# Kernel optimization log

Hardware: AMD Instinct MI355X
Metric: run time of the kernel (lower is better)

The kernel has to match this reference:

```python
import jax, jax.numpy as jnp
import numpy as np

B, CIN, H, W = 32, 10, 128, 128
APP, WIDTH, M1, M2 = 2, 64, 20, 20
NQ, NP, OUT, MID = 4, 2, 1, 128
LIFT = WIDTH - CIN - APP - NQ  # 48


def setup_inputs() -> dict:
    key = jax.random.key(0)
    ks = jax.random.split(key, 16)
    n = lambda k, s: jax.random.normal(k, s, dtype=jnp.float32)
    sc = 1.0 / (WIDTH * WIDTH)  # FNO spectral weight scale 1/(in*out)
    return {
        'x': n(ks[0], (B, CIN, H, W)),
        'qa': n(ks[1], (NQ, CIN + APP)) * 0.1,
        'qb': n(ks[2], (NQ, CIN + APP)) * 0.1,
        'fc0_w1': n(ks[3], (MID, CIN + APP + NQ)) * 0.1,
        'fc0_b1': jnp.zeros((MID,), jnp.float32),
        'fc0_w2': n(ks[4], (LIFT, MID)) * 0.1,
        'fc0_b2': jnp.zeros((LIFT,), jnp.float32),
        'sw1r': n(ks[5], (4, WIDTH, WIDTH, M1, M2)) * sc,
        'sw1i': n(ks[6], (4, WIDTH, WIDTH, M1, M2)) * sc,
        'sw2r': n(ks[7], (4, WIDTH, WIDTH, M1, M2)) * sc,
        'sw2i': n(ks[8], (4, WIDTH, WIDTH, M1, M2)) * sc,
        'cw': n(ks[9], (4, WIDTH, WIDTH, 3, 3)) * 0.05,
        'cb': jnp.zeros((4, WIDTH), jnp.float32),
        'pw': n(ks[10], (4, WIDTH, 2 * WIDTH + NP)) * 0.05,
        'pb': jnp.zeros((4, WIDTH), jnp.float32),
        'fc1_w1': n(ks[11], (MID, WIDTH)) * 0.1,
        'fc1_b1': jnp.zeros((MID,), jnp.float32),
        'fc1_w2': n(ks[12], (OUT, MID)) * 0.1,
        'fc1_b2': jnp.zeros((OUT,), jnp.float32),
    }


def _conv1x1(x, w, b):
    # x: (B,C,H,W), w: (O,C), b: (O,)
    return jnp.einsum('oc,bchw->bohw', w, x) + b[None, :, None, None]


def _spectral_conv(x, w1, w2):
    # standard FNO2d spectral conv: keep low modes in both rfft corners
    xf = jnp.fft.rfft2(x)                                  # (B,C,H,W//2+1) complex
    top = jnp.einsum('bixy,ioxy->boxy', xf[:, :, :M1, :M2], w1)
    bot = jnp.einsum('bixy,ioxy->boxy', xf[:, :, -M1:, :M2], w2)
    of = jnp.zeros((x.shape[0], WIDTH, H, W // 2 + 1), dtype=xf.dtype)
    of = of.at[:, :, :M1, :M2].set(top).at[:, :, -M1:, :M2].set(bot)
    return jnp.fft.irfft2(of, s=(H, W))


def _circ_conv3(x, w, b):
    # Conv2d(k=3, padding=1, padding_mode='circular')
    xp = jnp.pad(x, ((0, 0), (0, 0), (1, 1), (1, 1)), mode='wrap')
    y = jax.lax.conv_general_dilated(xp, w, (1, 1), 'VALID',
                                     dimension_numbers=('NCHW', 'OIHW', 'NCHW'))
    return y + b[None, :, None, None]


def _grid(b, h, w):
    gx = jnp.broadcast_to(jnp.linspace(0.0, 1.0, h, dtype=jnp.float32)[None, None, :, None], (b, 1, h, w))
    gy = jnp.broadcast_to(jnp.linspace(0.0, 1.0, w, dtype=jnp.float32)[None, None, None, :], (b, 1, h, w))
    return jnp.concatenate([gx, gy], axis=1)


def reference(x, qa, qb, fc0_w1, fc0_b1, fc0_w2, fc0_b2,
              sw1r, sw1i, sw2r, sw2i, cw, cb, pw, pb,
              fc1_w1, fc1_b1, fc1_w2, fc1_b2):
    b = x.shape[0]
    x = jnp.concatenate([x, _grid(b, H, W)], axis=1)            # (B, 12, H, W)
    # QuadPath (prep stage): product of two learned linear projections
    q = jnp.einsum('oc,bchw->bohw', qa, x) * jnp.einsum('oc,bchw->bohw', qb, x)
    x = jnp.concatenate([x, q], axis=1)                          # (B, 16, H, W)
    # fc0 lift MLP (1x1 conv -> gelu -> 1x1 conv), concat to reach width
    h0 = jax.nn.gelu(_conv1x1(x, fc0_w1, fc0_b1))
    x = jnp.concatenate([x, _conv1x1(h0, fc0_w2, fc0_b2)], axis=1)  # (B, 64, H, W)

    for i in range(4):
        x1 = _spectral_conv(x, sw1r[i] + 1j * sw1i[i], sw2r[i] + 1j * sw2i[i])
        x2 = _circ_conv3(x, cw[i], cb[i])
        xo = jnp.concatenate([x1, x2], axis=1)                   # (B, 128, H, W)
        prods = xo[:, :NP] * xo[:, NP:2 * NP]                     # ProductLayer pair products
        xo = _conv1x1(jnp.concatenate([xo, prods], axis=1), pw[i], pb[i])
        x = x + jnp.tanh(xo)

    h1 = jax.nn.gelu(_conv1x1(x, fc1_w1, fc1_b1))
    return _conv1x1(h1, fc1_w2, fc1_b2)                          # (B, 1, H, W)
```

## Files before the change

kernel.cpp:

```cpp
#include <hip/hip_runtime.h>
#include <math.h>

#define HW 16384

typedef __attribute__((ext_vector_type(8))) short short8;
typedef __attribute__((ext_vector_type(4))) float f32x4;
typedef unsigned int u32;

__device__ __forceinline__ float gelu_tanh(float x) {
    float x3 = x * x * x;
    float t = tanhf(0.7978845608028654f * (x + 0.044715f * x3));
    return 0.5f * x * (1.0f + t);
}

__device__ __forceinline__ u32 f2bf(float f) {
    u32 u = __builtin_bit_cast(u32, f);
    return (u + 0x7FFFu + ((u >> 16) & 1u)) >> 16;
}
__device__ __forceinline__ u32 pack2(float a, float b) {
    return f2bf(a) | (f2bf(b) << 16);
}

__global__ __launch_bounds__(256) void packw_kernel(
    const float* __restrict__ cw, short* __restrict__ wpk)
{
    int idx = blockIdx.x * 256 + threadIdx.x;
    if (idx >= 4 * 64 * 576) return;
    int L = idx / 36864, r = idx % 36864;
    int o = r / 576, k = r % 576;
    int tap = k >> 6, i = k & 63;
    wpk[idx] = (short)f2bf(cw[((size_t)(L * 64 + o) * 64 + i) * 9 + tap]);
}
__global__ __launch_bounds__(256) void packpw_kernel(
    const float* __restrict__ pw, short* __restrict__ pwk)
{
    int idx = blockIdx.x * 256 + threadIdx.x;
    if (idx >= 4 * 64 * 128) return;
    int L = idx >> 13, r = idx & 8191;
    int o = r >> 7, k = r & 127;
    pwk[idx] = (short)f2bf(pw[(size_t)L * 8320 + o * 130 + k]);
}
__global__ __launch_bounds__(256) void packfc_kernel(
    const float* __restrict__ fc0w1, const float* __restrict__ fc0w2,
    const float* __restrict__ fc1w1,
    short* __restrict__ w1k, short* __restrict__ w2k, short* __restrict__ f1wk)
{
    int i = blockIdx.x * 256 + threadIdx.x;
    if (i < 4096) {
        int m = i >> 5, k = i & 31;
        w1k[i] = (short)(k < 16 ? f2bf(fc0w1[m * 16 + k]) : 0);
    } else if (i < 10240) {
        int j = i - 4096; int o = j >> 7, m = j & 127;
        w2k[j] = (short)f2bf(fc0w2[o * 128 + m]);
    } else if (i < 18432) {
        int j = i - 10240; int m = j >> 6, c = j & 63;
        f1wk[j] = (short)f2bf(fc1w1[m * 64 + c]);
    }
}
__global__ __launch_bounds__(256) void packsw_kernel(
    const float* __restrict__ sw1r, const float* __restrict__ sw1i,
    const float* __restrict__ sw2r, const float* __restrict__ sw2i,
    u32* __restrict__ wswk)
{
    __shared__ short lr[64][202];
    __shared__ short li[64][202];
    int bi = blockIdx.x;
    int L = bi >> 7, i = (bi >> 1) & 63, kh = bi & 1;
    int t = threadIdx.x;
    int km0 = kh * 200;
    for (int region = 0; region < 2; ++region) {
        const float* srcR = region ? sw2r : sw1r;
        const float* srcI = region ? sw2i : sw1i;
        size_t sb = ((size_t)(L * 64 + i) * 64) * 400 + km0;
        for (int c = 0; c < 50; ++c) {
            int flat = c * 256 + t;
            int o = flat / 200, km = flat - o * 200;
            lr[o][km] = (short)f2bf(srcR[sb + (size_t)o * 400 + km]);
            li[o][km] = (short)f2bf(srcI[sb + (size_t)o * 400 + km]);
        }
        __syncthreads();
        u32* dst = wswk + ((size_t)L * 800 + (size_t)region * 400 + km0) * 4096 + (size_t)i * 64;
        for (int c = 0; c < 50; ++c) {
            int flat = c * 256 + t;
            int km = flat >> 6, o = flat & 63;
            dst[(size_t)km * 4096 + o] =
                (u32)(unsigned short)lr[o][km] | ((u32)(unsigned short)li[o][km] << 16);
        }
        __syncthreads();
    }
}
__global__ __launch_bounds__(256) void gen_dft_kernel(
    short* __restrict__ Wfg, short* __restrict__ Winvbg,
    short* __restrict__ Tfy, short* __restrict__ Tiy)
{
    int idx = blockIdx.x * 256 + threadIdx.x;
    if (idx < 6144) {
        int n = idx >> 7, xx = idx & 127;
        float val = 0.f;
        if (n < 40) {
            int kx = n >> 1;
            float s, c;
            sincosf(6.283185307179586f * (float)((kx * xx) & 127) / 128.0f, &s, &c);
            val = (n & 1) ? -s : c;
        }
        Wfg[idx] = (short)f2bf(val);
    } else if (idx < 14336) {
        int j = idx - 6144;
        int xx = j >> 6, k = j & 63;
        float val = 0.f;
        if (k < 40) {
            int kx = k >> 1;
            if (kx == 0) {
                val = (k & 1) ? 0.f : (1.0f / 16384.0f);
            } else {
                float s, c;
                sincosf(6.283185307179586f * (float)((kx * xx) & 127) / 128.0f, &s, &c);
                val = ((k & 1) ? -s : c) * (2.0f / 16384.0f);
            }
        }
        Winvbg[j] = (short)f2bf(val);
    } else if (idx < 24576) {
        int j = idx - 14336;
        int q = j >> 7, yy = j & 127;
        int kyi = q >> 1;
        int ky = kyi + ((kyi >= 20) ? 88 : 0);
        float s, c;
        sincosf(6.283185307179586f * (float)((ky * yy) & 127) / 128.0f, &s, &c);
        Tfy[j] = (short)f2bf((q & 1) ? s : c);
    } else if (idx < 36864) {
        int j = idx - 24576;
        int yy = j / 96, q = j - yy * 96;
        float val = 0.f;
        if (q < 80) {
            int kyi = q >> 1;
            int ky = kyi + ((kyi >= 20) ? 88 : 0);
            float s, c;
            sincosf(6.283185307179586f * (float)((ky * yy) & 127) / 128.0f, &s, &c);
            val = (q & 1) ? s : c;
        }
        Tiy[j] = (short)f2bf(val);
    }
}

__global__ __launch_bounds__(256) void front_mfma_kernel(
    const float* __restrict__ x,
    const float* __restrict__ qa, const float* __restrict__ qb,
    const short* __restrict__ w1k, const float* __restrict__ b1,
    const short* __restrict__ w2k, const float* __restrict__ b2,
    float* __restrict__ xbuf, short* __restrict__ xb16)
{
    __shared__ short V[128 * 40];
    __shared__ short A2[128 * 136];
    __shared__ float lqa[48], lqb[48], lb1[128], lb2[48];
    int t = threadIdx.x;
    int y = blockIdx.x, b = blockIdx.y;
    int lane = t & 63, w = t >> 6;

    if (t < 48) { lqa[t] = qa[t]; lqb[t] = qb[t]; lb2[t] = b2[t]; }
    if (t >= 128) lb1[t - 128] = b1[t - 128];
    __syncthreads();

    if (t < 128) {
        int xx = t;
        float v[16];
        const float* xsrc = x + (size_t)b * 10 * HW + y * 128 + xx;
#pragma unroll
        for (int c = 0; c < 10; ++c) v[c] = xsrc[c * HW];
        v[10] = (float)y * (1.0f / 127.0f);
        v[11] = (float)xx * (1.0f / 127.0f);
#pragma unroll
        for (int o = 0; o < 4; ++o) {
            float sa = 0.f, sb = 0.f;
#pragma unroll
            for (int c = 0; c < 12; ++c) { sa += lqa[o * 12 + c] * v[c]; sb += lqb[o * 12 + c] * v[c]; }
            v[12 + o] = sa * sb;
        }
        u32* vr = (u32*)&V[xx * 40];
#pragma unroll
        for (int j = 0; j < 8; ++j) vr[j] = pack2(v[2 * j], v[2 * j + 1]);
#pragma unroll
        for (int j = 8; j < 16; ++j) vr[j] = 0u;
        float* ob = xbuf + (size_t)b * 64 * HW + y * 128 + xx;
#pragma unroll
        for (int c = 0; c < 16; ++c) ob[(size_t)c * HW] = v[c];
        u32* hb = (u32*)&xb16[(((size_t)b * 128 + y) * 128 + xx) * 64];
#pragma unroll
        for (int j = 0; j < 8; ++j) hb[j] = vr[j];
    }
    __syncthreads();

    {
        short8 aF[2];
#pragma unroll
        for (int mi = 0; mi < 2; ++mi)
            aF[mi] = *(const short8*)(w1k + ((w * 2 + mi) * 16 + (lane & 15)) * 32 + (lane >> 4) * 8);
        f32x4 acc[2][8];
#pragma unroll
        for (int mi = 0; mi < 2; ++mi)
#pragma unroll
            for (int nf = 0; nf < 8; ++nf) acc[mi][nf] = (f32x4){0.f, 0.f, 0.f, 0.f};
#pragma unroll
        for (int nf = 0; nf < 8; ++nf) {
            int xx = nf * 16 + (lane & 15);
            short8 bF = *(const short8*)&V[xx * 40 + (lane >> 4) * 8];
#pragma unroll
            for (int mi = 0; mi < 2; ++mi)
                acc[mi][nf] = __builtin_amdgcn_mfma_f32_16x16x32_bf16(aF[mi], bF, acc[mi][nf], 0, 0, 0);
        }
#pragma unroll
        for (int mi = 0; mi < 2; ++mi) {
            int m0 = (w * 2 + mi) * 16 + (lane >> 4) * 4;
            float bb0 = lb1[m0], bb1 = lb1[m0 + 1], bb2 = lb1[m0 + 2], bb3 = lb1[m0 + 3];
#pragma unroll
            for (int nf = 0; nf < 8; ++nf) {
                int xx = nf * 16 + (lane & 15);
                float h0 = gelu_tanh(acc[mi][nf][0] + bb0);
                float h1 = gelu_tanh(acc[mi][nf][1] + bb1);
                float h2 = gelu_tanh(acc[mi][nf][2] + bb2);
                float h3 = gelu_tanh(acc[mi][nf][3] + bb3);
                *(int2*)&A2[xx * 136 + m0] = make_int2(pack2(h0, h1), pack2(h2, h3));
            }
        }
    }
    __syncthreads();

    {
        short8 aF[3][4];
#pragma unroll
        for (int mt = 0; mt < 3; ++mt)
#pragma unroll
            for (int ks = 0; ks < 4; ++ks)
                aF[mt][ks] = *(const short8*)(w2k + (mt * 16 + (lane & 15)) * 128 + ks * 32 + (lane >> 4) * 8);
#pragma unroll
        for (int ni = 0; ni < 2; ++ni) {
            int nt = w * 2 + ni;
            int xx = nt * 16 + (lane & 15);
            f32x4 acc[3];
#pragma unroll
            for (int mt = 0; mt < 3; ++mt) acc[mt] = (f32x4){0.f, 0.f, 0.f, 0.f};
#pragma unroll
            for (int ks = 0; ks < 4; ++ks) {
                short8 bF = *(const short8*)&A2[xx * 136 + ks * 32 + (lane >> 4) * 8];
#pragma unroll
                for (int mt = 0; mt < 3; ++mt)
                    acc[mt] = __builtin_amdgcn_mfma_f32_16x16x32_bf16(aF[mt][ks], bF, acc[mt], 0, 0, 0);
            }
#pragma unroll
            for (int mt = 0; mt < 3; ++mt) {
                int o0 = mt * 16 + (lane >> 4) * 4;
                float r0 = acc[mt][0] + lb2[o0], r1 = acc[mt][1] + lb2[o0 + 1];
                float r2 = acc[mt][2] + lb2[o0 + 2], r3 = acc[mt][3] + lb2[o0 + 3];
                float* ob = xbuf + (size_t)b * 64 * HW + (size_t)(16 + o0) * HW + y * 128 + xx;
                ob[0] = r0; ob[HW] = r1; ob[2 * HW] = r2; ob[3 * HW] = r3;
                *(int2*)&xb16[(((size_t)b * 128 + y) * 128 + xx) * 64 + 16 + o0] =
                    make_int2(pack2(r0, r1), pack2(r2, r3));
            }
        }
    }
}

__global__ __launch_bounds__(256) void dftfwd_kernel(
    const float* __restrict__ xin, const short* __restrict__ Wfg,
    const short* __restrict__ Tfy, float2* __restrict__ fm)
{
    __shared__ short img[128 * 128];
    __shared__ short S[48 * 140];
    int t = threadIdx.x;
    int bc = blockIdx.x;
    int lane = t & 63, w = t >> 6;

    const float* src = xin + (size_t)bc * HW;
#pragma unroll
    for (int i = 0; i < 8; ++i) {
        int chunk = i * 256 + t;
        int y = chunk >> 4, x8 = chunk & 15;
        const float* p = src + y * 128 + x8 * 8;
        f32x4 v0 = *(const f32x4*)p, v1 = *(const f32x4*)(p + 4);
        int4 h = make_int4(pack2(v0[0], v0[1]), pack2(v0[2], v0[3]),
                           pack2(v1[0], v1[1]), pack2(v1[2], v1[3]));
        *(int4*)&img[y * 128 + ((x8 ^ (y & 7)) << 3)] = h;
    }
    for (int z = t; z < 560; z += 256) ((u32*)S)[2800 + z] = 0u;

    short8 bF[3][4];
#pragma unroll
    for (int nf = 0; nf < 3; ++nf)
#pragma unroll
        for (int ks = 0; ks < 4; ++ks) {
            int n = nf * 16 + (lane & 15);
            bF[nf][ks] = *(const short8*)(Wfg + n * 128 + ks * 32 + (lane >> 4) * 8);
        }
    __syncthreads();

    {
        f32x4 acc[2][3];
#pragma unroll
        for (int a = 0; a < 2; ++a)
#pragma unroll
            for (int b2 = 0; b2 < 3; ++b2) acc[a][b2] = (f32x4){0.f, 0.f, 0.f, 0.f};
#pragma unroll
        for (int ks = 0; ks < 4; ++ks)
#pragma unroll
            for (int mf = 0; mf < 2; ++mf) {
                int y = w * 32 + mf * 16 + (lane & 15);
                int x0 = ks * 32 + (lane >> 4) * 8;
                short8 aF = *(const short8*)&img[y * 128 + ((((x0 >> 3) ^ (y & 7))) << 3)];
#pragma unroll
                for (int nf = 0; nf < 3; ++nf)
                    acc[mf][nf] = __builtin_amdgcn_mfma_f32_16x16x32_bf16(aF, bF[nf][ks], acc[mf][nf], 0, 0, 0);
            }
#pragma unroll
        for (int mf = 0; mf < 2; ++mf)
#pragma unroll
            for (int nf = 0; nf < 3; ++nf) {
                int n = nf * 16 + (lane & 15);
                if (n < 40) {
                    int y0 = w * 32 + mf * 16 + (lane >> 4) * 4;
                    *(int2*)&S[n * 140 + y0] = make_int2(pack2(acc[mf][nf][0], acc[mf][nf][1]),
                                                         pack2(acc[mf][nf][2], acc[mf][nf][3]));
                }
            }
    }
    __syncthreads();

    float2* fmo = fm + (size_t)bc * 800;
#pragma unroll
    for (int pi = 0; pi < 4; ++pi) {
        int p = w + pi * 4;
        if (p < 15) {
            int mt = p / 3, nt = p % 3;
            f32x4 acc = (f32x4){0.f, 0.f, 0.f, 0.f};
#pragma unroll
            for (int ks = 0; ks < 4; ++ks) {
                short8 aF = *(const short8*)(Tfy + (mt * 16 + (lane & 15)) * 128 + ks * 32 + (lane >> 4) * 8);
                short8 bG = *(const short8*)&S[(nt * 16 + (lane & 15)) * 140 + ks * 32 + (lane >> 4) * 8];
                acc = __builtin_amdgcn_mfma_f32_16x16x32_bf16(aF, bG, acc, 0, 0, 0);
            }
            float p0 = __shfl_xor(acc[0], 1), p1 = __shfl_xor(acc[1], 1);
            float p2 = __shfl_xor(acc[2], 1), p3 = __shfl_xor(acc[3], 1);
            int l15 = lane & 15;
            if (!(l15 & 1)) {
                int kx = nt * 8 + (l15 >> 1);
                if (kx < 20) {
                    int kyi0 = mt * 8 + ((lane >> 4) << 1);
                    fmo[kyi0 * 20 + kx] = make_float2(acc[0] + p1, p0 - acc[1]);
                    fmo[(kyi0 + 1) * 20 + kx] = make_float2(acc[2] + p3, p2 - acc[3]);
                }
            }
        }
    }
}

__global__ __launch_bounds__(256) void specmul_kernel(
    const float2* __restrict__ fm,
    const u32* __restrict__ wswk,
    float2* __restrict__ fm2, int nb64)
{
    __shared__ float2 lx[32 * 64];
    __shared__ u32 lw[64 * 64];
    int t = threadIdx.x;
    int mode = blockIdx.x;
    const u32* ws = wswk + (size_t)mode * 4096;
    for (int n = t; n < nb64; n += 256)
        lx[n] = fm[(size_t)n * 800 + mode];
    for (int n = t; n < 4096; n += 256)
        lw[n] = ws[n];
    __syncthreads();
    for (int n = t; n < nb64; n += 256) {
        int b = n >> 6, o = n & 63;
        float re = 0.f, imv = 0.f;
        const float2* xb = lx + b * 64;
#pragma unroll 8
        for (int i = 0; i < 64; ++i) {
            float2 a = xb[i];
            u32 wp = lw[i * 64 + o];
            float wr = __builtin_bit_cast(float, wp << 16);
            float wi = __builtin_bit_cast(float, wp & 0xffff0000u);
            re += a.x * wr - a.y * wi;
            imv += a.x * wi + a.y * wr;
        }
        fm2[(size_t)n * 800 + mode] = make_float2(re, imv);
    }
}

__global__ __launch_bounds__(256) void invA_mfma_kernel(
    const float2* __restrict__ fm2, const short* __restrict__ Tiy,
    short* __restrict__ g)
{
    __shared__ short F[48 * 104];
    int t = threadIdx.x;
    int bc = blockIdx.x;
    int lane = t & 63, w = t >> 6;
    int bb = bc >> 6, cc = bc & 63;
    u32* Fw = (u32*)F;
    const float2* src = fm2 + (size_t)bc * 800;
    for (int i = t; i < 800; i += 256) {
        float2 v = src[i];
        int kyi = i / 20, kx = i - kyi * 20;
        Fw[(2 * kx) * 52 + kyi]     = pack2(v.x, -v.y);
        Fw[(2 * kx + 1) * 52 + kyi] = pack2(v.y, v.x);
    }
    for (int i = t; i < 416; i += 256) Fw[2080 + i] = 0u;
    for (int i = t; i < 384; i += 256) {
        int n = i >> 3, k = i & 7;
        Fw[n * 52 + 40 + k] = 0u;
    }
    __syncthreads();

    short8 aF[3][3];
#pragma unroll
    for (int mt = 0; mt < 3; ++mt)
#pragma unroll
        for (int ks = 0; ks < 3; ++ks)
            aF[mt][ks] = *(const short8*)&F[(mt * 16 + (lane & 15)) * 104 + ks * 32 + (lane >> 4) * 8];

#pragma unroll
    for (int ni = 0; ni < 2; ++ni) {
        int nt = w * 2 + ni;
        int yy = nt * 16 + (lane & 15);
        short8 bF[3];
#pragma unroll
        for (int ks = 0; ks < 3; ++ks)
            bF[ks] = *(const short8*)(Tiy + yy * 96 + ks * 32 + (lane >> 4) * 8);
#pragma unroll
        for (int mt = 0; mt < 3; ++mt) {
            f32x4 acc = (f32x4){0.f, 0.f, 0.f, 0.f};
#pragma unroll
            for (int ks = 0; ks < 3; ++ks)
                acc = __builtin_amdgcn_mfma_f32_16x16x32_bf16(aF[mt][ks], bF[ks], acc, 0, 0, 0);
            int n0 = mt * 16 + (lane >> 4) * 4;
            *(int2*)&g[(((size_t)bb * 128 + yy) * 64 + cc) * 48 + n0] =
                make_int2(pack2(acc[0], acc[1]), pack2(acc[2], acc[3]));
        }
    }
}

__global__ __launch_bounds__(256) void invBcomb_kernel(
    const short* __restrict__ g,
    const short* __restrict__ Winvbg,
    const short* __restrict__ c2g,
    const short* __restrict__ pwk,
    const float* __restrict__ pw,
    const float* __restrict__ pb,
    float* __restrict__ xio,
    short* __restrict__ xb16)
{
    __shared__ short A[64 * 64];
    __shared__ short S1[128 * 64];
    __shared__ short C2[128 * 64];
    __shared__ float2 pr[128];
    int t = threadIdx.x;
    int y = blockIdx.x;
    int b = blockIdx.y;
    int lane = t & 63, w = t >> 6;
    short8 vz = {0, 0, 0, 0, 0, 0, 0, 0};

    {
        const short* gb = g + ((size_t)(b * 128 + y)) * 64 * 48;
#pragma unroll
        for (int i = 0; i < 2; ++i) {
            int chunk = i * 256 + t;
            int c = chunk >> 3, g8 = chunk & 7;
            short8 v = (g8 < 6) ? *(const short8*)(gb + c * 48 + g8 * 8) : vz;
            *(short8*)&A[(c << 6) + ((g8 ^ (c & 7)) << 3)] = v;
        }
    }
    {
        const short* c2b = c2g + ((size_t)(b * 128 + y)) * 128 * 64;
#pragma unroll
        for (int i = 0; i < 4; ++i) {
            int chunk = i * 256 + t;
            int xx = chunk >> 3, c8 = chunk & 7;
            *(short8*)&C2[xx * 64 + ((c8 ^ (xx & 7)) << 3)] = *(const short8*)(c2b + chunk * 8);
        }
    }
    short8 bFi[8][2];
#pragma unroll
    for (int nf = 0; nf < 8; ++nf)
#pragma unroll
        for (int ks = 0; ks < 2; ++ks) {
            int xx = nf * 16 + (lane & 15);
            bFi[nf][ks] = *(const short8*)(Winvbg + xx * 64 + ks * 32 + (lane >> 4) * 8);
        }
    __syncthreads();

    {
        int c0 = w * 16;
        int c = c0 + (lane & 15);
        int base = c << 6;
        short8 aF0 = *(const short8*)&A[base + (((lane >> 4) ^ (c & 7)) << 3)];
        short8 aF1 = *(const short8*)&A[base + (((4 + (lane >> 4)) ^ (c & 7)) << 3)];
        int cw = c0 + (lane >> 4) * 4;
        int swg = ((cw >> 3) & 7);
        int cwo = cw & 7;
        bool dopr = (w == 0) && ((lane >> 4) == 0);
#pragma unroll
        for (int nf = 0; nf < 8; ++nf) {
            f32x4 acc = (f32x4){0.f, 0.f, 0.f, 0.f};
            acc = __builtin_amdgcn_mfma_f32_16x16x32_bf16(aF0, bFi[nf][0], acc, 0, 0, 0);
            acc = __builtin_amdgcn_mfma_f32_16x16x32_bf16(aF1, bFi[nf][1], acc, 0, 0, 0);
            int xx = nf * 16 + (lane & 15);
            int dst = xx * 64 + ((swg ^ (xx & 7)) << 3) + cwo;
            *(int2*)&S1[dst] = make_int2(pack2(acc[0], acc[1]), pack2(acc[2], acc[3]));
            if (dopr) pr[xx] = make_float2(acc[0] * acc[2], acc[1] * acc[3]);
        }
    }

    short8 bFp[4][4];
#pragma unroll
    for (int nf = 0; nf < 4; ++nf)
#pragma unroll
        for (int ks = 0; ks < 4; ++ks) {
            int o = nf * 16 + (lane & 15);
            bFp[nf][ks] = *(const short8*)(pwk + o * 128 + ks * 32 + (lane >> 4) * 8);
        }
    __syncthreads();

    f32x4 acc[2][4];
#pragma unroll
    for (int a = 0; a < 2; ++a)
#pragma unroll
        for (int b2 = 0; b2 < 4; ++b2) acc[a][b2] = (f32x4){0.f, 0.f, 0.f, 0.f};

#pragma unroll
    for (int ks = 0; ks < 4; ++ks)
#pragma unroll
        for (int mf = 0; mf < 2; ++mf) {
            int xx = w * 32 + mf * 16 + (lane & 15);
            int k0 = ks * 32 + (lane >> 4) * 8;
            const short* src = (ks < 2) ? &S1[xx * 64 + ((((k0 >> 3) ^ (xx & 7))) << 3)]
                                        : &C2[xx * 64 + (((((k0 - 64) >> 3) ^ (xx & 7))) << 3)];
            short8 aF = *(const short8*)src;
#pragma unroll
            for (int nf = 0; nf < 4; ++nf)
                acc[mf][nf] = __builtin_amdgcn_mfma_f32_16x16x32_bf16(aF, bFp[nf][ks], acc[mf][nf], 0, 0, 0);
        }

#pragma unroll
    for (int mf = 0; mf < 2; ++mf) {
        int xr = w * 32 + mf * 16 + (lane >> 4) * 4;
        float2 prv0 = pr[xr], prv1 = pr[xr + 1], prv2 = pr[xr + 2], prv3 = pr[xr + 3];
#pragma unroll
        for (int nf = 0; nf < 4; ++nf) {
            int o = nf * 16 + (lane & 15);
            const float* pwrow = pw + o * 130;
            float pw128 = pwrow[128], pw129 = pwrow[129], pbv = pb[o];
            size_t off = ((size_t)(b * 64 + o)) * HW + y * 128 + xr;
            f32x4 xov = *(const f32x4*)(xio + off);
            f32x4 res;
            res[0] = xov[0] + tanhf(acc[mf][nf][0] + pbv + pw128 * prv0.x + pw129 * prv0.y);
            res[1] = xov[1] + tanhf(acc[mf][nf][1] + pbv + pw128 * prv1.x + pw129 * prv1.y);
            res[2] = xov[2] + tanhf(acc[mf][nf][2] + pbv + pw128 * prv2.x + pw129 * prv2.y);
            res[3] = xov[3] + tanhf(acc[mf][nf][3] + pbv + pw128 * prv3.x + pw129 * prv3.y);
            *(f32x4*)(xio + off) = res;
            size_t hbase = (((size_t)(b * 128 + y)) * 128 + xr) * 64 + o;
            xb16[hbase]       = (short)f2bf(res[0]);
            xb16[hbase + 64]  = (short)f2bf(res[1]);
            xb16[hbase + 128] = (short)f2bf(res[2]);
            xb16[hbase + 192] = (short)f2bf(res[3]);
        }
    }
}

__global__ __launch_bounds__(256) void conv3_mfma_kernel(
    const short* __restrict__ xb16,
    const short* __restrict__ wpk,
    const float* __restrict__ cb,
    short* __restrict__ c2g)
{
    __shared__ short xlds[3 * 128 * 64];
    int t = threadIdx.x;
    int y = blockIdx.x;
    int b = blockIdx.y;
    int lane = t & 63, wid = t >> 6;

    const short8* xs = (const short8*)(xb16 + ((size_t)b * 128) * 128 * 64);
#pragma unroll
    for (int i = 0; i < 12; ++i) {
        int c = i * 256 + t;
        int row = c >> 10;
        int rem = c & 1023;
        int xx = rem >> 3, i8 = rem & 7;
        int yy = (y + row + 127) & 127;
        short8 v = xs[((size_t)yy * 128 + xx) * 8 + i8];
        *(short8*)&xlds[(row * 128 + xx) * 64 + ((i8 ^ (xx & 7)) << 3)] = v;
    }

    int o0 = wid * 16;
    const short* wbase = wpk + (size_t)(o0 + (lane & 15)) * 576 + (lane >> 4) * 8;
    short8 aF[18];
#pragma unroll
    for (int s = 0; s < 18; ++s)
        aF[s] = *(const short8*)(wbase + s * 32);

    __syncthreads();

    f32x4 acc[8];
#pragma unroll
    for (int f = 0; f < 8; ++f) acc[f] = (f32x4){0.f, 0.f, 0.f, 0.f};
#pragma unroll
    for (int s = 0; s < 18; ++s) {
        const int tap = s >> 1;
        const int ky = tap / 3, kx = tap % 3;
        int ig = (s & 1) * 4 + (lane >> 4);
#pragma unroll
        for (int f = 0; f < 8; ++f) {
            int xx = (f * 16 + (lane & 15) + kx + 127) & 127;
            int off = (ky * 128 + xx) * 64 + ((ig ^ (xx & 7)) << 3);
            short8 bG = *(const short8*)&xlds[off];
            acc[f] = __builtin_amdgcn_mfma_f32_16x16x32_bf16(aF[s], bG, acc[f], 0, 0, 0);
        }
    }

    int ob = o0 + (lane >> 4) * 4;
    float bias0 = cb[ob], bias1 = cb[ob + 1], bias2 = cb[ob + 2], bias3 = cb[ob + 3];
    short* orow = c2g + ((size_t)(b * 128 + y)) * 128 * 64;
#pragma unroll
    for (int f = 0; f < 8; ++f) {
        int x = f * 16 + (lane & 15);
        *(int2*)&orow[x * 64 + ob] = make_int2(pack2(acc[f][0] + bias0, acc[f][1] + bias1),
                                               pack2(acc[f][2] + bias2, acc[f][3] + bias3));
    }
}

__global__ __launch_bounds__(256) void fc1_mfma_kernel(
    const short* __restrict__ xb16,
    const short* __restrict__ f1wk, const float* __restrict__ b1,
    const float* __restrict__ w2, const float* __restrict__ b2,
    float* __restrict__ out)
{
    __shared__ short X[128 * 72];
    __shared__ float lb1[128], lw2[128];
    int t = threadIdx.x;
    int y = blockIdx.x, b = blockIdx.y;
    int lane = t & 63, w = t >> 6;
    if (t < 128) { lb1[t] = b1[t]; lw2[t] = w2[t]; }
    const short8* src = (const short8*)(xb16 + (((size_t)b * 128 + y) * 128) * 64);
#pragma unroll
    for (int i = 0; i < 4; ++i) {
        int c = i * 256 + t;
        int xx = c >> 3, c8 = c & 7;
        *(short8*)&X[xx * 72 + ((c8 ^ (xx & 7)) << 3)] = src[c];
    }
    __syncthreads();

    float part0 = 0.f, part1 = 0.f;
#pragma unroll
    for (int mt = 0; mt < 8; ++mt) {
        short8 aF[2];
#pragma unroll
        for (int ks = 0; ks < 2; ++ks)
            aF[ks] = *(const short8*)(f1wk + (mt * 16 + (lane & 15)) * 64 + ks * 32 + (lane >> 4) * 8);
#pragma unroll
        for (int ni = 0; ni < 2; ++ni) {
            int xx = (w * 2 + ni) * 16 + (lane & 15);
            f32x4 acc = (f32x4){0.f, 0.f, 0.f, 0.f};
#pragma unroll
            for (int ks = 0; ks < 2; ++ks) {
                int g8 = ks * 4 + (lane >> 4);
                short8 bF = *(const short8*)&X[xx * 72 + ((g8 ^ (xx & 7)) << 3)];
                acc = __builtin_amdgcn_mfma_f32_16x16x32_bf16(aF[ks], bF, acc, 0, 0, 0);
            }
            int m0 = mt * 16 + (lane >> 4) * 4;
            float s = lw2[m0]     * gelu_tanh(acc[0] + lb1[m0])
                    + lw2[m0 + 1] * gelu_tanh(acc[1] + lb1[m0 + 1])
                    + lw2[m0 + 2] * gelu_tanh(acc[2] + lb1[m0 + 2])
                    + lw2[m0 + 3] * gelu_tanh(acc[3] + lb1[m0 + 3]);
            if (ni == 0) part0 += s; else part1 += s;
        }
    }
    part0 += __shfl_xor(part0, 16); part0 += __shfl_xor(part0, 32);
    part1 += __shfl_xor(part1, 16); part1 += __shfl_xor(part1, 32);
    if (lane < 16) {
        float bb = b2[0];
        out[(size_t)b * HW + y * 128 + (w * 2) * 16 + lane] = part0 + bb;
        out[(size_t)b * HW + y * 128 + (w * 2 + 1) * 16 + lane] = part1 + bb;
    }
}

extern "C" void kernel_launch(void* const* d_in, const int* in_sizes, int n_in,
                              void* d_out, int out_size, void* d_ws, size_t ws_size,
                              hipStream_t stream) {
    const float* x      = (const float*)d_in[0];
    const float* qa     = (const float*)d_in[1];
    const float* qb     = (const float*)d_in[2];
    const float* fc0w1  = (const float*)d_in[3];
    const float* fc0b1  = (const float*)d_in[4];
    const float* fc0w2  = (const float*)d_in[5];
    const float* fc0b2  = (const float*)d_in[6];
    const float* sw1r   = (const float*)d_in[7];
    const float* sw1i   = (const float*)d_in[8];
    const float* sw2r   = (const float*)d_in[9];
    const float* sw2i   = (const float*)d_in[10];
    const float* cw     = (const float*)d_in[11];
    const float* cb     = (const float*)d_in[12];
    const float* pw     = (const float*)d_in[13];
    const float* pb     = (const float*)d_in[14];
    const float* fc1w1  = (const float*)d_in[15];
    const float* fc1b1  = (const float*)d_in[16];
    const float* fc1w2  = (const float*)d_in[17];
    const float* fc1b2  = (const float*)d_in[18];

    const size_t WPK_F = 73728, PWK_F = 16384, WFG_F = 3072, WIB_F = 4096;
    const size_t TFY_F = 5120, TIY_F = 6144, FCK_F = 9216;
    const size_t WSW_F = 13107200;
    const size_t CONST_F = WPK_F + PWK_F + WFG_F + WIB_F + TFY_F + TIY_F + FCK_F + WSW_F;
    const size_t PER_B_F = 1048576u + 2u * 524288u + 196608u + 2u * 102400u;
    int NB = 32;
    while (NB > 1 && ((size_t)NB * PER_B_F + CONST_F) * 4 > ws_size) NB >>= 1;
    if (((size_t)NB * PER_B_F + CONST_F) * 4 > ws_size) return;

    float* fb = (float*)d_ws;
    short* wpk    = (short*)fb;                 fb += WPK_F;
    short* pwk    = (short*)fb;                 fb += PWK_F;
    short* Wfg    = (short*)fb;                 fb += WFG_F;
    short* Winvbg = (short*)fb;                 fb += WIB_F;
    short* Tfy    = (short*)fb;                 fb += TFY_F;
    short* Tiy    = (short*)fb;                 fb += TIY_F;
    short* w1k    = (short*)fb;
    short* w2k    = w1k + 4096;
    short* f1wk   = w1k + 10240;                fb += FCK_F;
    u32*   wswk   = (u32*)fb;                   fb += WSW_F;

    float*  xA    = fb;
    short*  xb16  = (short*)(xA + (size_t)NB * 1048576u);
    short*  c2g   = xb16 + (size_t)NB * 1048576u;
    short*  g     = c2g + (size_t)NB * 1048576u;
    float2* fm    = (float2*)(g + (size_t)NB * 393216u);
    float2* fm2   = fm + (size_t)NB * 51200u;

    packw_kernel<<<576, 256, 0, stream>>>(cw, wpk);
    packpw_kernel<<<128, 256, 0, stream>>>(pw, pwk);
    packfc_kernel<<<72, 256, 0, stream>>>(fc0w1, fc0w2, fc1w1, w1k, w2k, f1wk);
    gen_dft_kernel<<<144, 256, 0, stream>>>(Wfg, Winvbg, Tfy, Tiy);
    packsw_kernel<<<512, 256, 0, stream>>>(sw1r, sw1i, sw2r, sw2i, wswk);

    for (int b0 = 0; b0 < 32; b0 += NB) {
        front_mfma_kernel<<<dim3(128, NB), 256, 0, stream>>>(
            x + (size_t)b0 * 10 * HW, qa, qb, w1k, fc0b1, w2k, fc0b2, xA, xb16);

        for (int L = 0; L < 4; ++L) {
            dftfwd_kernel<<<NB * 64, 256, 0, stream>>>(xA, Wfg, Tfy, fm);
            specmul_kernel<<<800, 256, 0, stream>>>(fm, wswk + (size_t)L * 800 * 4096,
                                                    fm2, NB * 64);
            invA_mfma_kernel<<<NB * 64, 256, 0, stream>>>(fm2, Tiy, g);
            conv3_mfma_kernel<<<dim3(128, NB), 256, 0, stream>>>(
                xb16, wpk + (size_t)L * 36864, cb + (size_t)L * 64, c2g);
            invBcomb_kernel<<<dim3(128, NB), 256, 0, stream>>>(
                g, Winvbg, c2g, pwk + (size_t)L * 8192, pw + (size_t)L * 8320,
                pb + (size_t)L * 64, xA, xb16);
        }

        fc1_mfma_kernel<<<dim3(128, NB), 256, 0, stream>>>(
            xb16, f1wk, fc1b1, fc1w2, fc1b2, (float*)d_out + (size_t)b0 * HW);
    }
}
```

Measured before the change: 1.545 ms.

## Fuse circular 3x3 conv into inverse-DFT combine kernel with ping-pong bf16 buffers

Result: faster. 1.462 ms (-5.3%).

```diff
diff --git a/kernel.cpp b/kernel.cpp
--- a/kernel.cpp
+++ b/kernel.cpp
@@ -435,26 +435,39 @@
     }
 }
 
-__global__ __launch_bounds__(256) void invBcomb_kernel(
+__global__ __launch_bounds__(256) void convcomb_kernel(
+    const short* __restrict__ xb16o,
+    const short* __restrict__ wpk,
+    const float* __restrict__ cb,
     const short* __restrict__ g,
     const short* __restrict__ Winvbg,
-    const short* __restrict__ c2g,
     const short* __restrict__ pwk,
     const float* __restrict__ pw,
     const float* __restrict__ pb,
     float* __restrict__ xio,
-    short* __restrict__ xb16)
-{
+    short* __restrict__ xb16n)
+{
+    __shared__ short xlds[3 * 128 * 64];
     __shared__ short A[64 * 64];
     __shared__ short S1[128 * 64];
-    __shared__ short C2[128 * 64];
     __shared__ float2 pr[128];
     int t = threadIdx.x;
     int y = blockIdx.x;
     int b = blockIdx.y;
-    int lane = t & 63, w = t >> 6;
+    int lane = t & 63, wid = t >> 6;
     short8 vz = {0, 0, 0, 0, 0, 0, 0, 0};
 
+    const short8* xs = (const short8*)(xb16o + ((size_t)b * 128) * 128 * 64);
+#pragma unroll
+    for (int i = 0; i < 12; ++i) {
+        int c = i * 256 + t;
+        int row = c >> 10;
+        int rem = c & 1023;
+        int xx = rem >> 3, i8 = rem & 7;
+        int yy = (y + row + 127) & 127;
+        short8 v = xs[((size_t)yy * 128 + xx) * 8 + i8];
+        *(short8*)&xlds[(row * 128 + xx) * 64 + ((i8 ^ (xx & 7)) << 3)] = v;
+    }
     {
         const short* gb = g + ((size_t)(b * 128 + y)) * 64 * 48;
 #pragma unroll
@@ -465,27 +478,42 @@
             *(short8*)&A[(c << 6) + ((g8 ^ (c & 7)) << 3)] = v;
         }
     }
+    int o0 = wid * 16;
+    const short* wbase = wpk + (size_t)(o0 + (lane & 15)) * 576 + (lane >> 4) * 8;
+    short8 aFc[18];
+#pragma unroll
+    for (int s = 0; s < 18; ++s)
+        aFc[s] = *(const short8*)(wbase + s * 32);
+
+    __syncthreads();
+
+    f32x4 accC[8];
+#pragma unroll
+    for (int f = 0; f < 8; ++f) accC[f] = (f32x4){0.f, 0.f, 0.f, 0.f};
+#pragma unroll
+    for (int s = 0; s < 18; ++s) {
+        const int tap = s >> 1;
+        const int ky = tap / 3, kx = tap % 3;
+        int ig = (s & 1) * 4 + (lane >> 4);
+#pragma unroll
+        for (int f = 0; f < 8; ++f) {
+            int xx = (f * 16 + (lane & 15) + kx + 127) & 127;
+            int off = (ky * 128 + xx) * 64 + ((ig ^ (xx & 7)) << 3);
+            short8 bG = *(const short8*)&xlds[off];
+            accC[f] = __builtin_amdgcn_mfma_f32_16x16x32_bf16(aFc[s], bG, accC[f], 0, 0, 0);
+        }
+    }
+
     {
-        const short* c2b = c2g + ((size_t)(b * 128 + y)) * 128 * 64;
-#pragma unroll
-        for (int i = 0; i < 4; ++i) {
-            int chunk = i * 256 + t;
-            int xx = chunk >> 3, c8 = chunk & 7;
-            *(short8*)&C2[xx * 64 + ((c8 ^ (xx & 7)) << 3)] = *(const short8*)(c2b + chunk * 8);
-        }
-    }
-    short8 bFi[8][2];
-#pragma unroll
-    for (int nf = 0; nf < 8; ++nf)
-#pragma unroll
-        for (int ks = 0; ks < 2; ++ks) {
-            int xx = nf * 16 + (lane & 15);
-            bFi[nf][ks] = *(const short8*)(Winvbg + xx * 64 + ks * 32 + (lane >> 4) * 8);
-        }
-    __syncthreads();
-
-    {
-        int c0 = w * 16;
+        short8 bFi[8][2];
+#pragma unroll
+        for (int nf = 0; nf < 8; ++nf)
+#pragma unroll
+            for (int ks = 0; ks < 2; ++ks) {
+                int xx = nf * 16 + (lane & 15);
+                bFi[nf][ks] = *(const short8*)(Winvbg + xx * 64 + ks * 32 + (lane >> 4) * 8);
+            }
+        int c0 = wid * 16;
         int c = c0 + (lane & 15);
         int base = c << 6;
         short8 aF0 = *(const short8*)&A[base + (((lane >> 4) ^ (c & 7)) << 3)];
@@ -493,7 +521,7 @@
         int cw = c0 + (lane >> 4) * 4;
         int swg = ((cw >> 3) & 7);
         int cwo = cw & 7;
-        bool dopr = (w == 0) && ((lane >> 4) == 0);
+        bool dopr = (wid == 0) && ((lane >> 4) == 0);
 #pragma unroll
         for (int nf = 0; nf < 8; ++nf) {
             f32x4 acc = (f32x4){0.f, 0.f, 0.f, 0.f};
@@ -506,6 +534,22 @@
         }
     }
 
+    __syncthreads();
+
+    short* C2 = xlds;
+    {
+        int ob = o0 + (lane >> 4) * 4;
+        float bias0 = cb[ob], bias1 = cb[ob + 1], bias2 = cb[ob + 2], bias3 = cb[ob + 3];
+        int swg = ((ob >> 3) & 7);
+        int cwo = ob & 7;
+#pragma unroll
+        for (int f = 0; f < 8; ++f) {
+            int x = f * 16 + (lane & 15);
+            int dst = x * 64 + ((swg ^ (x & 7)) << 3) + cwo;
+            *(int2*)&C2[dst] = make_int2(pack2(accC[f][0] + bias0, accC[f][1] + bias1),
+                                         pack2(accC[f][2] + bias2, accC[f][3] + bias3));
+        }
+    }
     short8 bFp[4][4];
 #pragma unroll
     for (int nf = 0; nf < 4; ++nf)
@@ -526,7 +570,7 @@
     for (int ks = 0; ks < 4; ++ks)
 #pragma unroll
         for (int mf = 0; mf < 2; ++mf) {
-            int xx = w * 32 + mf * 16 + (lane & 15);
+            int xx = wid * 32 + mf * 16 + (lane & 15);
             int k0 = ks * 32 + (lane >> 4) * 8;
             const short* src = (ks < 2) ? &S1[xx * 64 + ((((k0 >> 3) ^ (xx & 7))) << 3)]
                                         : &C2[xx * 64 + (((((k0 - 64) >> 3) ^ (xx & 7))) << 3)];
@@ -538,7 +582,7 @@
 
 #pragma unroll
     for (int mf = 0; mf < 2; ++mf) {
-        int xr = w * 32 + mf * 16 + (lane >> 4) * 4;
+        int xr = wid * 32 + mf * 16 + (lane >> 4) * 4;
         float2 prv0 = pr[xr], prv1 = pr[xr + 1], prv2 = pr[xr + 2], prv3 = pr[xr + 3];
 #pragma unroll
         for (int nf = 0; nf < 4; ++nf) {
@@ -554,72 +598,11 @@
             res[3] = xov[3] + tanhf(acc[mf][nf][3] + pbv + pw128 * prv3.x + pw129 * prv3.y);
             *(f32x4*)(xio + off) = res;
             size_t hbase = (((size_t)(b * 128 + y)) * 128 + xr) * 64 + o;
-            xb16[hbase]       = (short)f2bf(res[0]);
-            xb16[hbase + 64]  = (short)f2bf(res[1]);
-            xb16[hbase + 128] = (short)f2bf(res[2]);
-            xb16[hbase + 192] = (short)f2bf(res[3]);
-        }
-    }
-}
-
-__global__ __launch_bounds__(256) void conv3_mfma_kernel(
-    const short* __restrict__ xb16,
-    const short* __restrict__ wpk,
-    const float* __restrict__ cb,
-    short* __restrict__ c2g)
-{
-    __shared__ short xlds[3 * 128 * 64];
-    int t = threadIdx.x;
-    int y = blockIdx.x;
-    int b = blockIdx.y;
-    int lane = t & 63, wid = t >> 6;
-
-    const short8* xs = (const short8*)(xb16 + ((size_t)b * 128) * 128 * 64);
-#pragma unroll
-    for (int i = 0; i < 12; ++i) {
-        int c = i * 256 + t;
-        int row = c >> 10;
-        int rem = c & 1023;
-        int xx = rem >> 3, i8 = rem & 7;
-        int yy = (y + row + 127) & 127;
-        short8 v = xs[((size_t)yy * 128 + xx) * 8 + i8];
-        *(short8*)&xlds[(row * 128 + xx) * 64 + ((i8 ^ (xx & 7)) << 3)] = v;
-    }
-
-    int o0 = wid * 16;
-    const short* wbase = wpk + (size_t)(o0 + (lane & 15)) * 576 + (lane >> 4) * 8;
-    short8 aF[18];
-#pragma unroll
-    for (int s = 0; s < 18; ++s)
-        aF[s] = *(const short8*)(wbase + s * 32);
-
-    __syncthreads();
-
-    f32x4 acc[8];
-#pragma unroll
-    for (int f = 0; f < 8; ++f) acc[f] = (f32x4){0.f, 0.f, 0.f, 0.f};
-#pragma unroll
-    for (int s = 0; s < 18; ++s) {
-        const int tap = s >> 1;
-        const int ky = tap / 3, kx = tap % 3;
-        int ig = (s & 1) * 4 + (lane >> 4);
-#pragma unroll
-        for (int f = 0; f < 8; ++f) {
-            int xx = (f * 16 + (lane & 15) + kx + 127) & 127;
-            int off = (ky * 128 + xx) * 64 + ((ig ^ (xx & 7)) << 3);
-            short8 bG = *(const short8*)&xlds[off];
-            acc[f] = __builtin_amdgcn_mfma_f32_16x16x32_bf16(aF[s], bG, acc[f], 0, 0, 0);
-        }
-    }
-
-    int ob = o0 + (lane >> 4) * 4;
-    float bias0 = cb[ob], bias1 = cb[ob + 1], bias2 = cb[ob + 2], bias3 = cb[ob + 3];
-    short* orow = c2g + ((size_t)(b * 128 + y)) * 128 * 64;
-#pragma unroll
-    for (int f = 0; f < 8; ++f) {
-        int x = f * 16 + (lane & 15);
-        *(int2*)&orow[x * 64 + ob] = make_int2(pack2(acc[f][0] + bias0, acc[f][1] + bias1),
-                                               pack2(acc[f][2] + bias2, acc[f][3] + bias3));
+            xb16n[hbase]       = (short)f2bf(res[0]);
+            xb16n[hbase + 64]  = (short)f2bf(res[1]);
+            xb16n[hbase + 128] = (short)f2bf(res[2]);
+            xb16n[hbase + 192] = (short)f2bf(res[3]);
+        }
     }
 }
 
@@ -723,9 +706,9 @@
     u32*   wswk   = (u32*)fb;                   fb += WSW_F;
 
     float*  xA    = fb;
-    short*  xb16  = (short*)(xA + (size_t)NB * 1048576u);
-    short*  c2g   = xb16 + (size_t)NB * 1048576u;
-    short*  g     = c2g + (size_t)NB * 1048576u;
+    short*  xb16A = (short*)(xA + (size_t)NB * 1048576u);
+    short*  xb16B = xb16A + (size_t)NB * 1048576u;
+    short*  g     = xb16B + (size_t)NB * 1048576u;
     float2* fm    = (float2*)(g + (size_t)NB * 393216u);
     float2* fm2   = fm + (size_t)NB * 51200u;
 
@@ -737,21 +720,23 @@
 
     for (int b0 = 0; b0 < 32; b0 += NB) {
         front_mfma_kernel<<<dim3(128, NB), 256, 0, stream>>>(
-            x + (size_t)b0 * 10 * HW, qa, qb, w1k, fc0b1, w2k, fc0b2, xA, xb16);
-
+            x + (size_t)b0 * 10 * HW, qa, qb, w1k, fc0b1, w2k, fc0b2, xA, xb16A);
+
+        short* xo = xb16A;
+        short* xn = xb16B;
         for (int L = 0; L < 4; ++L) {
             dftfwd_kernel<<<NB * 64, 256, 0, stream>>>(xA, Wfg, Tfy, fm);
             specmul_kernel<<<800, 256, 0, stream>>>(fm, wswk + (size_t)L * 800 * 4096,
                                                     fm2, NB * 64);
             invA_mfma_kernel<<<NB * 64, 256, 0, stream>>>(fm2, Tiy, g);
-            conv3_mfma_kernel<<<dim3(128, NB), 256, 0, stream>>>(
-                xb16, wpk + (size_t)L * 36864, cb + (size_t)L * 64, c2g);
-            invBcomb_kernel<<<dim3(128, NB), 256, 0, stream>>>(
-                g, Winvbg, c2g, pwk + (size_t)L * 8192, pw + (size_t)L * 8320,
-                pb + (size_t)L * 64, xA, xb16);
+            convcomb_kernel<<<dim3(128, NB), 256, 0, stream>>>(
+                xo, wpk + (size_t)L * 36864, cb + (size_t)L * 64,
+                g, Winvbg, pwk + (size_t)L * 8192, pw + (size_t)L * 8320,
+                pb + (size_t)L * 64, xA, xn);
+            short* tmp = xo; xo = xn; xn = tmp;
         }
 
         fc1_mfma_kernel<<<dim3(128, NB), 256, 0, stream>>>(
-            xb16, f1wk, fc1b1, fc1w2, fc1b2, (float*)d_out + (size_t)b0 * HW);
-    }
-}
+            xo, f1wk, fc1b1, fc1w2, fc1b2, (float*)d_out + (size_t)b0 * HW);
+    }
+}
```
